# Performance work log

Measured on AMD Instinct MI355X. Metric: run time of the kernel, lower is better.

Reference implementation:

```python
import jax, jax.numpy as jnp
import numpy as np

N_DATA = 131072
N_HID = 32768
D = 256
E1 = 524288  # data -> hidden
E2 = 524288  # hidden -> hidden
E3 = 524288  # hidden -> data


def setup_inputs() -> dict:
    key = jax.random.key(0)
    ks = jax.random.split(key, 32)
    rn = lambda k, shape, s=0.05: (jax.random.normal(k, shape, jnp.float32) * s)
    inp = {
        "data_x": jax.random.normal(ks[0], (N_DATA, 8), jnp.float32),
        "hidden_x": jax.random.normal(ks[1], (N_HID, 3), jnp.float32),
        "dh_src": jax.random.randint(ks[2], (E1,), 0, N_DATA, jnp.int32),
        "dh_dst": jax.random.randint(ks[3], (E1,), 0, N_HID, jnp.int32),
        "hh_src": jax.random.randint(ks[4], (E2,), 0, N_HID, jnp.int32),
        "hh_dst": jax.random.randint(ks[5], (E2,), 0, N_HID, jnp.int32),
        "hd_src": jax.random.randint(ks[6], (E3,), 0, N_HID, jnp.int32),
        "hd_dst": jax.random.randint(ks[7], (E3,), 0, N_DATA, jnp.int32),
        # encoder params
        "enc_src_w": rn(ks[8], (D, 8)), "enc_src_b": rn(ks[9], (D,)),
        "enc_dst_w": rn(ks[10], (D, 3)), "enc_dst_b": rn(ks[11], (D,)),
        "enc_wl": rn(ks[12], (D, D)), "enc_bl": rn(ks[13], (D,)), "enc_wr": rn(ks[14], (D, D)),
        # processor params
        "proc_wl": rn(ks[15], (D, D)), "proc_bl": rn(ks[16], (D,)), "proc_wr": rn(ks[17], (D, D)),
        "proc_mlp_w": rn(ks[18], (D, D)), "proc_mlp_b": rn(ks[19], (D,)),
        # decoder params
        "dec_src_w": rn(ks[20], (D, D)), "dec_src_b": rn(ks[21], (D,)),
        "dec_dst_w": rn(ks[22], (D, 8)), "dec_dst_b": rn(ks[23], (D,)),
        "dec_wl": rn(ks[24], (D, D)), "dec_bl": rn(ks[25], (D,)), "dec_wr": rn(ks[26], (D, D)),
        "out_w": rn(ks[27], (8, D)), "out_b": rn(ks[28], (8,)),
    }
    return inp


def _gelu(x):
    return jax.nn.gelu(x, approximate=False)  # torch nn.GELU default (erf)


def _sage(x_src, x_dst, src, dst, wl, bl, wr, n_dst):
    """PyG SAGEConv, mean aggregation: lin_l(mean_j x_src[j]) + lin_r(x_dst)."""
    msg = x_src[src]                                              # [E, D] gather
    agg = jax.ops.segment_sum(msg, dst, num_segments=n_dst)       # [n_dst, D]
    cnt = jax.ops.segment_sum(jnp.ones((src.shape[0], 1), msg.dtype), dst,
                              num_segments=n_dst)
    mean = agg / jnp.maximum(cnt, 1.0)
    return mean @ wl.T + bl + x_dst @ wr.T


def reference(data_x, hidden_x, dh_src, dh_dst, hh_src, hh_dst, hd_src, hd_dst,
              enc_src_w, enc_src_b, enc_dst_w, enc_dst_b, enc_wl, enc_bl, enc_wr,
              proc_wl, proc_bl, proc_wr, proc_mlp_w, proc_mlp_b,
              dec_src_w, dec_src_b, dec_dst_w, dec_dst_b, dec_wl, dec_bl, dec_wr,
              out_w, out_b):
    # ---- encoder: data -> hidden ----
    h_data = _gelu(data_x @ enc_src_w.T + enc_src_b)
    h_hid = _gelu(hidden_x @ enc_dst_w.T + enc_dst_b)
    h_hid = _gelu(_sage(h_data, h_hid, dh_src, dh_dst, enc_wl, enc_bl, enc_wr, N_HID))
    # ---- processor: hidden -> hidden, then GELU-Linear-GELU MLP ----
    h_hid = _sage(h_hid, h_hid, hh_src, hh_dst, proc_wl, proc_bl, proc_wr, N_HID)
    h_hid = _gelu(_gelu(h_hid) @ proc_mlp_w.T + proc_mlp_b)
    # ---- decoder: hidden -> data ----
    s = _gelu(h_hid @ dec_src_w.T + dec_src_b)
    d = _gelu(data_x @ dec_dst_w.T + dec_dst_b)
    d = _gelu(_sage(s, d, hd_src, hd_dst, dec_wl, dec_bl, dec_wr, N_DATA))
    return d @ out_w.T + out_b  # [N_DATA, 8]
```

## Files before the change

kernel.cpp:

```cpp
#include <hip/hip_runtime.h>
#include <stdint.h>

#define NDATA 131072
#define NHID  32768
#define NEDGE 524288

typedef __bf16 bf16_t;
typedef __bf16 bf16x4 __attribute__((ext_vector_type(4)));
typedef __bf16 bf16x8 __attribute__((ext_vector_type(8)));
typedef float  f32x4  __attribute__((ext_vector_type(4)));

__device__ __forceinline__ float gelu_f(float x) {
    return 0.5f * x * (1.0f + erff(x * 0.7071067811865476f));
}

__device__ __forceinline__ void glds16(const void* g, void* l) {
    auto* gp = reinterpret_cast<const __attribute__((address_space(1))) uint32_t*>(
        reinterpret_cast<uintptr_t>(g));
    auto* lp = reinterpret_cast<__attribute__((address_space(3))) uint32_t*>(
        reinterpret_cast<uintptr_t>(l));
    __builtin_amdgcn_global_load_lds(gp, lp, 16, 0, 0);
}

struct WPtrs { const float* p[10]; };

__global__ __launch_bounds__(256)
void cvt_w_kernel(WPtrs wp, bf16_t* __restrict__ out) {
    const int i = blockIdx.x * 256 + threadIdx.x;
    if (i < 8 * 65536) {
        const int wsel = i >> 16, off = i & 65535;
        out[i] = (bf16_t)wp.p[wsel][off];
    } else if (i < 8 * 65536 + 2048) {
        out[i] = (bf16_t)wp.p[8][i - 8 * 65536];
    } else {
        out[i] = (bf16_t)wp.p[9][i - (8 * 65536 + 2048)];
    }
}

struct EdgePtrs { const int* src[3]; const int* dst[3]; };

__device__ __forceinline__ int cnt_off_of(int g) { return g == 0 ? 0 : (g == 1 ? NHID : 2 * NHID); }
__device__ __forceinline__ int rp_off_of(int g)  { return g == 0 ? 0 : (g == 1 ? NHID + 1 : 2 * NHID + 2); }
__device__ __forceinline__ int shift_of(int g)   { return g == 2 ? 10 : 8; }

__global__ __launch_bounds__(256)
void hist3(EdgePtrs ep, int* __restrict__ cnt_all) {
    const int g = blockIdx.x >> 11;
    const int i = ((blockIdx.x & 2047) << 8) + threadIdx.x;
    atomicAdd(&cnt_all[cnt_off_of(g) + ep.dst[g][i]], 1);
}

__global__ __launch_bounds__(256)
void scan_blk3(const int* __restrict__ cnt_all, int* __restrict__ pre_all,
               int* __restrict__ blk) {
    __shared__ int sh[256];
    const int bid = blockIdx.x;
    int g, local;
    if (bid < 32)      { g = 0; local = bid; }
    else if (bid < 64) { g = 1; local = bid - 32; }
    else               { g = 2; local = bid - 64; }
    const int t = threadIdx.x;
    const int cbase = cnt_off_of(g) + local * 1024 + t * 4;
    const int pbase = rp_off_of(g)  + local * 1024 + t * 4;
    int4 v = *(const int4*)(cnt_all + cbase);
    sh[t] = v.x + v.y + v.z + v.w;
    __syncthreads();
    for (int off = 1; off < 256; off <<= 1) {
        int other = 0;
        if (t >= off) other = sh[t - off];
        __syncthreads();
        if (t >= off) sh[t] += other;
        __syncthreads();
    }
    const int excl = (t == 0) ? 0 : sh[t - 1];
    int4 o;
    o.x = excl; o.y = o.x + v.x; o.z = o.y + v.y; o.w = o.z + v.z;
    *(int4*)(pre_all + pbase) = o;
    if (t == 255) blk[bid] = sh[255];
}

__global__ __launch_bounds__(256)
void scan_add3(const int* __restrict__ pre_all, const int* __restrict__ blk,
               int* __restrict__ rp_all, int* __restrict__ binA) {
    __shared__ int sh[256];
    const int bid = blockIdx.x;
    int g, local, gbase;
    if (bid < 32)      { g = 0; local = bid;      gbase = 0; }
    else if (bid < 64) { g = 1; local = bid - 32; gbase = 32; }
    else               { g = 2; local = bid - 64; gbase = 64; }
    const int t = threadIdx.x;
    int part = 0;
    if (t < local) part = blk[gbase + t];
    sh[t] = part;
    __syncthreads();
    for (int o2 = 128; o2 > 0; o2 >>= 1) {
        if (t < o2) sh[t] += sh[t + o2];
        __syncthreads();
    }
    const int off = sh[0];
    const int idx = local * 1024 + t * 4;
    const int pbase = rp_off_of(g) + idx;
    int4 v = *(const int4*)(pre_all + pbase);
    v.x += off; v.y += off; v.z += off; v.w += off;
    *(int4*)(rp_all + pbase) = v;
    const int bw = 1 << shift_of(g);
    if ((idx & (bw - 1)) == 0) binA[g * 128 + (idx >> shift_of(g))] = v.x;
    if (local == 0 && t == 0) {
        const int n = (g == 2) ? NDATA : NHID;
        rp_all[rp_off_of(g) + n] = NEDGE;
    }
}

__global__ __launch_bounds__(256)
void partition3(EdgePtrs ep, int* __restrict__ binA, int2* __restrict__ pairs) {
    __shared__ int hist[128], base[128], cur[128];
    const int g = blockIdx.x >> 7;
    const int blk = blockIdx.x & 127;
    const int t = threadIdx.x;
    const int shift = shift_of(g);
    const int e_base = blk * 4096;
    const int* src = ep.src[g];
    const int* dst = ep.dst[g];
    if (t < 128) { hist[t] = 0; cur[t] = 0; }
    __syncthreads();
    #pragma unroll
    for (int it = 0; it < 16; ++it) {
        const int d = dst[e_base + it * 256 + t];
        atomicAdd(&hist[d >> shift], 1);
    }
    __syncthreads();
    if (t < 128) base[t] = atomicAdd(&binA[g * 128 + t], hist[t]);
    __syncthreads();
    #pragma unroll
    for (int it = 0; it < 16; ++it) {
        const int e = e_base + it * 256 + t;
        const int s = src[e], d = dst[e];
        const int b = d >> shift;
        const int l = atomicAdd(&cur[b], 1);
        pairs[(size_t)g * NEDGE + base[b] + l] = make_int2(s, d);
    }
}

__global__ __launch_bounds__(256)
void binsort3(const int2* __restrict__ pairs, const int* __restrict__ rp_all,
              int* __restrict__ sorted_all) {
    __shared__ int cur[1024];
    const int g = blockIdx.x >> 7;
    const int b = blockIdx.x & 127;
    const int t = threadIdx.x;
    const int shift = shift_of(g);
    const int W = 1 << shift;
    const int d0 = b << shift;
    const int rpo = rp_off_of(g);
    for (int i = t; i < W; i += 256) cur[i] = rp_all[rpo + d0 + i];
    __syncthreads();
    const int e0 = rp_all[rpo + d0];
    const int e1 = rp_all[rpo + d0 + W];
    for (int e = e0 + t; e < e1; e += 256) {
        const int2 p = pairs[(size_t)g * NEDGE + e];
        const int pos = atomicAdd(&cur[p.y - d0], 1);
        sorted_all[(size_t)g * NEDGE + pos] = p.x;
    }
}

__global__ __launch_bounds__(256)
void csr_gather_mean(const bf16_t* __restrict__ feat, const int* __restrict__ row_ptr,
                     const int* __restrict__ sorted_src, bf16_t* __restrict__ mean, int n) {
    const int lane = threadIdx.x & 63;
    const int half = lane >> 5;
    const int col8 = (lane & 31) * 8;
    const int w = blockIdx.x * 4 + (threadIdx.x >> 6);
    if (w >= n) return;
    const int e0 = row_ptr[w], e1 = row_ptr[w + 1];
    float acc[8] = {0.f, 0.f, 0.f, 0.f, 0.f, 0.f, 0.f, 0.f};
    int e = e0 + half;
    for (; e + 2 < e1; e += 4) {
        const int s0 = sorted_src[e], s1 = sorted_src[e + 2];
        const bf16x8 v0 = *(const bf16x8*)(feat + (size_t)s0 * 256 + col8);
        const bf16x8 v1 = *(const bf16x8*)(feat + (size_t)s1 * 256 + col8);
        #pragma unroll
        for (int j = 0; j < 8; ++j) acc[j] += (float)v0[j] + (float)v1[j];
    }
    for (; e < e1; e += 2) {
        const int s0 = sorted_src[e];
        const bf16x8 v0 = *(const bf16x8*)(feat + (size_t)s0 * 256 + col8);
        #pragma unroll
        for (int j = 0; j < 8; ++j) acc[j] += (float)v0[j];
    }
    #pragma unroll
    for (int j = 0; j < 8; ++j) acc[j] += __shfl_xor(acc[j], 32, 64);
    if (half == 0) {
        const float ic = 1.0f / fmaxf((float)(e1 - e0), 1.0f);
        bf16x8 r;
        #pragma unroll
        for (int j = 0; j < 8; ++j) r[j] = (bf16_t)(acc[j] * ic);
        *(bf16x8*)(mean + (size_t)w * 256 + col8) = r;
    }
}

__global__ __launch_bounds__(256)
void enc_both(const float* __restrict__ hx, const float* __restrict__ w3,
              const float* __restrict__ b3, bf16_t* __restrict__ out3,
              const float* __restrict__ dx, const float* __restrict__ w8,
              const float* __restrict__ b8, bf16_t* __restrict__ out8) {
    __shared__ float ws[8 * 256];
    __shared__ float bs[256];
    const int t = threadIdx.x;
    const bool is8 = (blockIdx.x >= 512);
    if (is8) {
        #pragma unroll
        for (int j = 0; j < 8; ++j) ws[j * 256 + t] = w8[t * 8 + j];
        bs[t] = b8[t];
    } else {
        #pragma unroll
        for (int j = 0; j < 3; ++j) ws[j * 256 + t] = w3[t * 3 + j];
        bs[t] = b3[t];
    }
    __syncthreads();
    const int lane = t & 63, wv = t >> 6;
    const int f0 = lane * 4;
    const float4 b4 = *(const float4*)(&bs[f0]);
    if (!is8) {
        for (int node = blockIdx.x * 4 + wv; node < NHID; node += 512 * 4) {
            const float* xr = hx + (size_t)node * 3;
            float xv[3];
            #pragma unroll
            for (int j = 0; j < 3; ++j) xv[j] = xr[j];
            float a0 = b4.x, a1 = b4.y, a2 = b4.z, a3 = b4.w;
            #pragma unroll
            for (int j = 0; j < 3; ++j) {
                const float4 w4 = *(const float4*)(&ws[j * 256 + f0]);
                a0 += xv[j] * w4.x; a1 += xv[j] * w4.y;
                a2 += xv[j] * w4.z; a3 += xv[j] * w4.w;
            }
            bf16x4 r;
            r[0] = (bf16_t)gelu_f(a0); r[1] = (bf16_t)gelu_f(a1);
            r[2] = (bf16_t)gelu_f(a2); r[3] = (bf16_t)gelu_f(a3);
            *(bf16x4*)(out3 + (size_t)node * 256 + f0) = r;
        }
    } else {
        for (int node = (blockIdx.x - 512) * 4 + wv; node < NDATA; node += 2048 * 4) {
            const float* xr = dx + (size_t)node * 8;
            float xv[8];
            #pragma unroll
            for (int j = 0; j < 8; ++j) xv[j] = xr[j];
            float a0 = b4.x, a1 = b4.y, a2 = b4.z, a3 = b4.w;
            #pragma unroll
            for (int j = 0; j < 8; ++j) {
                const float4 w4 = *(const float4*)(&ws[j * 256 + f0]);
                a0 += xv[j] * w4.x; a1 += xv[j] * w4.y;
                a2 += xv[j] * w4.z; a3 += xv[j] * w4.w;
            }
            bf16x4 r;
            r[0] = (bf16_t)gelu_f(a0); r[1] = (bf16_t)gelu_f(a1);
            r[2] = (bf16_t)gelu_f(a2); r[3] = (bf16_t)gelu_f(a3);
            *(bf16x4*)(out8 + (size_t)node * 256 + f0) = r;
        }
    }
}

template<int DUAL>
__global__ __launch_bounds__(256, 4)
void mfma_gemm(const bf16_t* __restrict__ A1, const bf16_t* __restrict__ W1,
               const bf16_t* __restrict__ A2, const bf16_t* __restrict__ W2,
               const float* __restrict__ bias, bf16_t* __restrict__ C) {
    __shared__ bf16_t As[8 * 64 * 8];
    __shared__ bf16_t Bs[8 * 256 * 8];
    const int t = threadIdx.x;
    const int w = t >> 6, lane = t & 63;
    const int l15 = lane & 15, l4 = lane >> 4;
    const int m0 = blockIdx.x * 64;

    f32x4 acc[4][4];
    #pragma unroll
    for (int nb = 0; nb < 4; ++nb) {
        const float bv = bias[w * 64 + nb * 16 + l15];
        #pragma unroll
        for (int m = 0; m < 4; ++m) {
            acc[m][nb][0] = bv; acc[m][nb][1] = bv; acc[m][nb][2] = bv; acc[m][nb][3] = bv;
        }
    }

    #pragma unroll
    for (int p = 0; p <= DUAL; ++p) {
        const bf16_t* Ap = p ? A2 : A1;
        const bf16_t* Wp = p ? W2 : W1;
        for (int kt = 0; kt < 4; ++kt) {
            const int k0 = kt * 64;
            __syncthreads();
            glds16(Ap + (size_t)(m0 + lane) * 256 + k0 + w * 8, &As[(w * 64) * 8]);
            glds16(Ap + (size_t)(m0 + lane) * 256 + k0 + (w + 4) * 8, &As[((w + 4) * 64) * 8]);
            #pragma unroll
            for (int q = 0; q < 8; ++q)
                glds16(Wp + (size_t)(w * 64 + lane) * 256 + k0 + q * 8,
                       &Bs[(q * 256 + w * 64) * 8]);
            __syncthreads();
            #pragma unroll
            for (int h = 0; h < 2; ++h) {
                bf16x8 af[4], bfr[4];
                #pragma unroll
                for (int m = 0; m < 4; ++m)
                    af[m] = *(const bf16x8*)(&As[((h * 4 + l4) * 64 + m * 16 + l15) * 8]);
                #pragma unroll
                for (int nb = 0; nb < 4; ++nb)
                    bfr[nb] = *(const bf16x8*)(&Bs[((h * 4 + l4) * 256 + w * 64 + nb * 16 + l15) * 8]);
                #pragma unroll
                for (int m = 0; m < 4; ++m)
                    #pragma unroll
                    for (int nb = 0; nb < 4; ++nb)
                        acc[m][nb] = __builtin_amdgcn_mfma_f32_16x16x32_bf16(af[m], bfr[nb], acc[m][nb], 0, 0, 0);
            }
        }
    }

    #pragma unroll
    for (int m = 0; m < 4; ++m) {
        #pragma unroll
        for (int nb = 0; nb < 4; ++nb) {
            const int col = w * 64 + nb * 16 + l15;
            #pragma unroll
            for (int i = 0; i < 4; ++i) {
                const int row = m0 + m * 16 + l4 * 4 + i;
                C[(size_t)row * 256 + col] = (bf16_t)gelu_f(acc[m][nb][i]);
            }
        }
    }
}

__global__ __launch_bounds__(256, 4)
void dec_gemm(const bf16_t* __restrict__ A1, const bf16_t* __restrict__ W1,
              const float* __restrict__ xdat, const bf16_t* __restrict__ wdb,
              const float* __restrict__ bd, const bf16_t* __restrict__ W2,
              const float* __restrict__ bias, const bf16_t* __restrict__ owb,
              const float* __restrict__ ob, float* __restrict__ out) {
    __shared__ __align__(16) char smem[40960];
    bf16_t* As   = (bf16_t*)smem;
    bf16_t* Bs   = (bf16_t*)(smem + 8192);
    bf16_t* tt   = (bf16_t*)smem;
    float*  part = (float*)(smem + 16384);

    const int t = threadIdx.x;
    const int w = t >> 6, lane = t & 63;
    const int l15 = lane & 15, l4 = lane >> 4;
    const int m0 = blockIdx.x * 64;

    bf16x8 af_x;
    #pragma unroll
    for (int j = 0; j < 8; ++j) af_x[j] = (bf16_t)0.0f;
    if (l4 == 0) {
        const float* xrp = xdat + (size_t)(m0 + w * 16 + l15) * 8;
        const float4 xa = *(const float4*)(xrp);
        const float4 xb = *(const float4*)(xrp + 4);
        af_x[0] = (bf16_t)xa.x; af_x[1] = (bf16_t)xa.y; af_x[2] = (bf16_t)xa.z; af_x[3] = (bf16_t)xa.w;
        af_x[4] = (bf16_t)xb.x; af_x[5] = (bf16_t)xb.y; af_x[6] = (bf16_t)xb.z; af_x[7] = (bf16_t)xb.w;
    }

    f32x4 acc[4][4];
    #pragma unroll
    for (int nb = 0; nb < 4; ++nb) {
        const float bv = bias[w * 64 + nb * 16 + l15];
        #pragma unroll
        for (int m = 0; m < 4; ++m) {
            acc[m][nb][0] = bv; acc[m][nb][1] = bv; acc[m][nb][2] = bv; acc[m][nb][3] = bv;
        }
    }

    #pragma unroll
    for (int p = 0; p < 2; ++p) {
        const bf16_t* Wp = p ? W2 : W1;
        for (int kt = 0; kt < 4; ++kt) {
            const int k0 = kt * 64;
            __syncthreads();
            if (p == 0) {
                glds16(A1 + (size_t)(m0 + lane) * 256 + k0 + w * 8, &As[(w * 64) * 8]);
                glds16(A1 + (size_t)(m0 + lane) * 256 + k0 + (w + 4) * 8, &As[((w + 4) * 64) * 8]);
            } else {
                #pragma unroll
                for (int nb2 = 0; nb2 < 4; ++nb2) {
                    const int cl = nb2 * 16 + l15;
                    const int col = k0 + cl;
                    f32x4 ad;
                    const float bv = bd[col];
                    ad[0] = bv; ad[1] = bv; ad[2] = bv; ad[3] = bv;
                    bf16x8 bf_d;
                    #pragma unroll
                    for (int j = 0; j < 8; ++j) bf_d[j] = (bf16_t)0.0f;
                    if (l4 == 0) bf_d = *(const bf16x8*)(wdb + col * 8);
                    ad = __builtin_amdgcn_mfma_f32_16x16x32_bf16(af_x, bf_d, ad, 0, 0, 0);
                    const int kq = cl >> 3, jj = cl & 7;
                    #pragma unroll
                    for (int i = 0; i < 4; ++i)
                        As[(kq * 64 + w * 16 + l4 * 4 + i) * 8 + jj] = (bf16_t)gelu_f(ad[i]);
                }
            }
            #pragma unroll
            for (int q = 0; q < 8; ++q)
                glds16(Wp + (size_t)(w * 64 + lane) * 256 + k0 + q * 8,
                       &Bs[(q * 256 + w * 64) * 8]);
            __syncthreads();
            #pragma unroll
            for (int h = 0; h < 2; ++h) {
                bf16x8 af[4], bfr[4];
                #pragma unroll
                for (int m = 0; m < 4; ++m)
                    af[m] = *(const bf16x8*)(&As[((h * 4 + l4) * 64 + m * 16 + l15) * 8]);
                #pragma unroll
                for (int nb = 0; nb < 4; ++nb)
                    bfr[nb] = *(const bf16x8*)(&Bs[((h * 4 + l4) * 256 + w * 64 + nb * 16 + l15) * 8]);
                #pragma unroll
                for (int m = 0; m < 4; ++m)
                    #pragma unroll
                    for (int nb = 0; nb < 4; ++nb)
                        acc[m][nb] = __builtin_amdgcn_mfma_f32_16x16x32_bf16(af[m], bfr[nb], acc[m][nb], 0, 0, 0);
            }
        }
    }

    __syncthreads();

    bf16x8 owf[2];
    #pragma unroll
    for (int s = 0; s < 2; ++s) {
        #pragma unroll
        for (int j = 0; j < 8; ++j) owf[s][j] = (bf16_t)0.0f;
        if (l15 < 8)
            owf[s] = *(const bf16x8*)(owb + l15 * 256 + w * 64 + s * 32 + l4 * 8);
    }

    bf16_t* ttw = tt + w * 2048;
    #pragma unroll
    for (int h = 0; h < 2; ++h) {
        #pragma unroll
        for (int mm = 0; mm < 2; ++mm) {
            const int m = h * 2 + mm;
            #pragma unroll
            for (int nb = 0; nb < 4; ++nb) {
                const int col = nb * 16 + l15;
                const int kg = col >> 3, cj = col & 7;
                #pragma unroll
                for (int i = 0; i < 4; ++i) {
                    const int rl = mm * 16 + l4 * 4 + i;
                    ttw[(kg * 32 + rl) * 8 + cj] = (bf16_t)gelu_f(acc[m][nb][i]);
                }
            }
        }
        f32x4 accp[2];
        #pragma unroll
        for (int mb = 0; mb < 2; ++mb) {
            accp[mb][0] = 0.f; accp[mb][1] = 0.f; accp[mb][2] = 0.f; accp[mb][3] = 0.f;
            #pragma unroll
            for (int s = 0; s < 2; ++s) {
                const bf16x8 af = *(const bf16x8*)(&ttw[((s * 4 + l4) * 32 + mb * 16 + l15) * 8]);
                accp[mb] = __builtin_amdgcn_mfma_f32_16x16x32_bf16(af, owf[s], accp[mb], 0, 0, 0);
            }
        }
        __syncthreads();
        #pragma unroll
        for (int mb = 0; mb < 2; ++mb)
            #pragma unroll
            for (int i = 0; i < 4; ++i)
                part[(w * 32 + mb * 16 + l4 * 4 + i) * 16 + l15] = accp[mb][i];
        __syncthreads();
        {
            const int row = t >> 3, o = t & 7;
            const float v = part[(0 * 32 + row) * 16 + o] + part[(1 * 32 + row) * 16 + o]
                          + part[(2 * 32 + row) * 16 + o] + part[(3 * 32 + row) * 16 + o] + ob[o];
            out[(size_t)(m0 + h * 32 + row) * 8 + o] = v;
        }
    }
}


extern "C" void kernel_launch(void* const* d_in, const int* in_sizes, int n_in,
                              void* d_out, int out_size, void* d_ws, size_t ws_size,
                              hipStream_t stream) {
    const float* data_x   = (const float*)d_in[0];
    const float* hidden_x = (const float*)d_in[1];
    const int* dh_src = (const int*)d_in[2];
    const int* dh_dst = (const int*)d_in[3];
    const int* hh_src = (const int*)d_in[4];
    const int* hh_dst = (const int*)d_in[5];
    const int* hd_src = (const int*)d_in[6];
    const int* hd_dst = (const int*)d_in[7];
    const float* enc_src_w = (const float*)d_in[8];
    const float* enc_src_b = (const float*)d_in[9];
    const float* enc_dst_w = (const float*)d_in[10];
    const float* enc_dst_b = (const float*)d_in[11];
    const float* enc_wl = (const float*)d_in[12];
    const float* enc_bl = (const float*)d_in[13];
    const float* enc_wr = (const float*)d_in[14];
    const float* proc_wl = (const float*)d_in[15];
    const float* proc_bl = (const float*)d_in[16];
    const float* proc_wr = (const float*)d_in[17];
    const float* proc_mlp_w = (const float*)d_in[18];
    const float* proc_mlp_b = (const float*)d_in[19];
    const float* dec_src_w = (const float*)d_in[20];
    const float* dec_src_b = (const float*)d_in[21];
    const float* dec_dst_w = (const float*)d_in[22];
    const float* dec_dst_b = (const float*)d_in[23];
    const float* dec_wl = (const float*)d_in[24];
    const float* dec_bl = (const float*)d_in[25];
    const float* dec_wr = (const float*)d_in[26];
    const float* out_w  = (const float*)d_in[27];
    const float* out_b  = (const float*)d_in[28];
    float* out = (float*)d_out;

    bf16_t* h_a   = (bf16_t*)d_ws;
    bf16_t* h_b   = h_a + (size_t)NHID * 256;
    bf16_t* h_msg = h_b + (size_t)NHID * 256;
    bf16_t* dmean = h_msg + (size_t)NDATA * 256;
    bf16_t* wbuf  = dmean + (size_t)NDATA * 256;
    int* cnt_all    = (int*)(wbuf + 8 * 65536 + 4096);
    int* rp_all     = cnt_all + (2 * NHID + NDATA);
    int* sorted_all = rp_all + (2 * NHID + NDATA + 3);
    int* blk_sums   = sorted_all + (size_t)3 * NEDGE;
    int* binA       = blk_sums + 192;
    int2* pairs     = (int2*)(((uintptr_t)(binA + 384) + 15) & ~(uintptr_t)15);

    bf16_t* W_enc_wl  = wbuf + 0 * 65536;
    bf16_t* W_enc_wr  = wbuf + 1 * 65536;
    bf16_t* W_proc_wl = wbuf + 2 * 65536;
    bf16_t* W_proc_wr = wbuf + 3 * 65536;
    bf16_t* W_mlp     = wbuf + 4 * 65536;
    bf16_t* W_dec_src = wbuf + 5 * 65536;
    bf16_t* W_dec_wl  = wbuf + 6 * 65536;
    bf16_t* W_dec_wr  = wbuf + 7 * 65536;
    bf16_t* W_out     = wbuf + 8 * 65536;
    bf16_t* W_dd      = wbuf + 8 * 65536 + 2048;

    const int* rp_dh = rp_all;
    const int* rp_hh = rp_all + NHID + 1;
    const int* rp_hd = rp_all + 2 * NHID + 2;
    const int* so_dh = sorted_all;
    const int* so_hh = sorted_all + NEDGE;
    const int* so_hd = sorted_all + 2 * (size_t)NEDGE;

    WPtrs wp;
    wp.p[0] = enc_wl;  wp.p[1] = enc_wr;  wp.p[2] = proc_wl; wp.p[3] = proc_wr;
    wp.p[4] = proc_mlp_w; wp.p[5] = dec_src_w; wp.p[6] = dec_wl; wp.p[7] = dec_wr;
    wp.p[8] = out_w; wp.p[9] = dec_dst_w;
    cvt_w_kernel<<<2064, 256, 0, stream>>>(wp, wbuf);

    EdgePtrs ep;
    ep.src[0] = dh_src; ep.dst[0] = dh_dst;
    ep.src[1] = hh_src; ep.dst[1] = hh_dst;
    ep.src[2] = hd_src; ep.dst[2] = hd_dst;
    hipMemsetAsync(cnt_all, 0, (size_t)(2 * NHID + NDATA) * sizeof(int), stream);
    hist3<<<3 * 2048, 256, 0, stream>>>(ep, cnt_all);
    scan_blk3<<<192, 256, 0, stream>>>(cnt_all, rp_all, blk_sums);
    scan_add3<<<192, 256, 0, stream>>>(rp_all, blk_sums, rp_all, binA);
    partition3<<<3 * 128, 256, 0, stream>>>(ep, binA, pairs);
    binsort3<<<3 * 128, 256, 0, stream>>>(pairs, rp_all, sorted_all);

    enc_both<<<2560, 256, 0, stream>>>(hidden_x, enc_dst_w, enc_dst_b, h_a,
                                       data_x, enc_src_w, enc_src_b, h_msg);
    csr_gather_mean<<<NHID / 4, 256, 0, stream>>>(h_msg, rp_dh, so_dh, h_b, NHID);
    mfma_gemm<1><<<NHID / 64, 256, 0, stream>>>(h_b, W_enc_wl, h_a, W_enc_wr, enc_bl, h_b);

    csr_gather_mean<<<NHID / 4, 256, 0, stream>>>(h_b, rp_hh, so_hh, h_a, NHID);
    mfma_gemm<1><<<NHID / 64, 256, 0, stream>>>(h_a, W_proc_wl, h_b, W_proc_wr, proc_bl, h_a);
    mfma_gemm<0><<<NHID / 64, 256, 0, stream>>>(h_a, W_mlp, nullptr, nullptr, proc_mlp_b, h_b);
    mfma_gemm<0><<<NHID / 64, 256, 0, stream>>>(h_b, W_dec_src, nullptr, nullptr, dec_src_b, h_a);

    csr_gather_mean<<<NDATA / 4, 256, 0, stream>>>(h_a, rp_hd, so_hd, dmean, NDATA);
    dec_gemm<<<NDATA / 64, 256, 0, stream>>>(dmean, W_dec_wl, data_x, W_dd, dec_dst_b,
                                             W_dec_wr, dec_bl, W_out, out_b, out);
}
```

Measured before the change: 482.9 us.

## Drop block barriers in MFMA GEMMs via wave-private weight staging and direct A loads

The GEMM kernels now load A fragments straight from global memory into registers. Each wave stages only its own weight slice in LDS with a per-wave vmcnt fence, which removes the per-step __syncthreads. mfma_gemm halves its row tile to 32 so twice as many blocks launch, and uses a 32-wide K step. dec_gemm precomputes the whole data_x encoder tile into LDS up front instead of per K step, at the cost of more shared memory and occupancy lowered to 3. Without block barriers, the in-place GEMMs (C aliasing A1) can race: one wave may write output rows while another wave is still reading them.

```diff
diff --git a/kernel.cpp b/kernel.cpp
--- a/kernel.cpp
+++ b/kernel.cpp
@@ -20,6 +20,11 @@
     auto* lp = reinterpret_cast<__attribute__((address_space(3))) uint32_t*>(
         reinterpret_cast<uintptr_t>(l));
     __builtin_amdgcn_global_load_lds(gp, lp, 16, 0, 0);
+}
+
+__device__ __forceinline__ void wave_vm_fence() {
+    asm volatile("s_waitcnt vmcnt(0)" ::: "memory");
+    __builtin_amdgcn_sched_barrier(0);
 }
 
 struct WPtrs { const float* p[10]; };
@@ -264,19 +269,18 @@
 void mfma_gemm(const bf16_t* __restrict__ A1, const bf16_t* __restrict__ W1,
                const bf16_t* __restrict__ A2, const bf16_t* __restrict__ W2,
                const float* __restrict__ bias, bf16_t* __restrict__ C) {
-    __shared__ bf16_t As[8 * 64 * 8];
-    __shared__ bf16_t Bs[8 * 256 * 8];
+    __shared__ bf16_t Bs[4 * 256 * 8];
     const int t = threadIdx.x;
     const int w = t >> 6, lane = t & 63;
     const int l15 = lane & 15, l4 = lane >> 4;
-    const int m0 = blockIdx.x * 64;
-
-    f32x4 acc[4][4];
+    const int m0 = blockIdx.x * 32;
+
+    f32x4 acc[2][4];
     #pragma unroll
     for (int nb = 0; nb < 4; ++nb) {
         const float bv = bias[w * 64 + nb * 16 + l15];
         #pragma unroll
-        for (int m = 0; m < 4; ++m) {
+        for (int m = 0; m < 2; ++m) {
             acc[m][nb][0] = bv; acc[m][nb][1] = bv; acc[m][nb][2] = bv; acc[m][nb][3] = bv;
         }
     }
@@ -285,36 +289,32 @@
     for (int p = 0; p <= DUAL; ++p) {
         const bf16_t* Ap = p ? A2 : A1;
         const bf16_t* Wp = p ? W2 : W1;
-        for (int kt = 0; kt < 4; ++kt) {
-            const int k0 = kt * 64;
-            __syncthreads();
-            glds16(Ap + (size_t)(m0 + lane) * 256 + k0 + w * 8, &As[(w * 64) * 8]);
-            glds16(Ap + (size_t)(m0 + lane) * 256 + k0 + (w + 4) * 8, &As[((w + 4) * 64) * 8]);
-            #pragma unroll
-            for (int q = 0; q < 8; ++q)
+        for (int kt = 0; kt < 8; ++kt) {
+            const int k0 = kt * 32;
+            __builtin_amdgcn_sched_barrier(0);
+            #pragma unroll
+            for (int q = 0; q < 4; ++q)
                 glds16(Wp + (size_t)(w * 64 + lane) * 256 + k0 + q * 8,
                        &Bs[(q * 256 + w * 64) * 8]);
-            __syncthreads();
-            #pragma unroll
-            for (int h = 0; h < 2; ++h) {
-                bf16x8 af[4], bfr[4];
-                #pragma unroll
-                for (int m = 0; m < 4; ++m)
-                    af[m] = *(const bf16x8*)(&As[((h * 4 + l4) * 64 + m * 16 + l15) * 8]);
+            bf16x8 af[2];
+            #pragma unroll
+            for (int m = 0; m < 2; ++m)
+                af[m] = *(const bf16x8*)(Ap + (size_t)(m0 + m * 16 + l15) * 256 + k0 + l4 * 8);
+            wave_vm_fence();
+            bf16x8 bfr[4];
+            #pragma unroll
+            for (int nb = 0; nb < 4; ++nb)
+                bfr[nb] = *(const bf16x8*)(&Bs[(l4 * 256 + w * 64 + nb * 16 + l15) * 8]);
+            #pragma unroll
+            for (int m = 0; m < 2; ++m)
                 #pragma unroll
                 for (int nb = 0; nb < 4; ++nb)
-                    bfr[nb] = *(const bf16x8*)(&Bs[((h * 4 + l4) * 256 + w * 64 + nb * 16 + l15) * 8]);
-                #pragma unroll
-                for (int m = 0; m < 4; ++m)
-                    #pragma unroll
-                    for (int nb = 0; nb < 4; ++nb)
-                        acc[m][nb] = __builtin_amdgcn_mfma_f32_16x16x32_bf16(af[m], bfr[nb], acc[m][nb], 0, 0, 0);
-            }
-        }
-    }
-
-    #pragma unroll
-    for (int m = 0; m < 4; ++m) {
+                    acc[m][nb] = __builtin_amdgcn_mfma_f32_16x16x32_bf16(af[m], bfr[nb], acc[m][nb], 0, 0, 0);
+        }
+    }
+
+    #pragma unroll
+    for (int m = 0; m < 2; ++m) {
         #pragma unroll
         for (int nb = 0; nb < 4; ++nb) {
             const int col = w * 64 + nb * 16 + l15;
@@ -327,15 +327,15 @@
     }
 }
 
-__global__ __launch_bounds__(256, 4)
+__global__ __launch_bounds__(256, 3)
 void dec_gemm(const bf16_t* __restrict__ A1, const bf16_t* __restrict__ W1,
               const float* __restrict__ xdat, const bf16_t* __restrict__ wdb,
               const float* __restrict__ bd, const bf16_t* __restrict__ W2,
               const float* __restrict__ bias, const bf16_t* __restrict__ owb,
               const float* __restrict__ ob, float* __restrict__ out) {
-    __shared__ __align__(16) char smem[40960];
-    bf16_t* As   = (bf16_t*)smem;
-    bf16_t* Bs   = (bf16_t*)(smem + 8192);
+    __shared__ __align__(16) char smem[49152];
+    bf16_t* dL = (bf16_t*)smem;
+    bf16_t* Bs = (bf16_t*)(smem + 32768);
     bf16_t* tt   = (bf16_t*)smem;
     float*  part = (float*)(smem + 16384);
 
@@ -344,15 +344,33 @@
     const int l15 = lane & 15, l4 = lane >> 4;
     const int m0 = blockIdx.x * 64;
 
-    bf16x8 af_x;
-    #pragma unroll
-    for (int j = 0; j < 8; ++j) af_x[j] = (bf16_t)0.0f;
-    if (l4 == 0) {
-        const float* xrp = xdat + (size_t)(m0 + w * 16 + l15) * 8;
-        const float4 xa = *(const float4*)(xrp);
-        const float4 xb = *(const float4*)(xrp + 4);
-        af_x[0] = (bf16_t)xa.x; af_x[1] = (bf16_t)xa.y; af_x[2] = (bf16_t)xa.z; af_x[3] = (bf16_t)xa.w;
-        af_x[4] = (bf16_t)xb.x; af_x[5] = (bf16_t)xb.y; af_x[6] = (bf16_t)xb.z; af_x[7] = (bf16_t)xb.w;
+    {
+        bf16x8 af_x;
+        #pragma unroll
+        for (int j = 0; j < 8; ++j) af_x[j] = (bf16_t)0.0f;
+        if (l4 == 0) {
+            const float* xrp = xdat + (size_t)(m0 + w * 16 + l15) * 8;
+            const float4 xa = *(const float4*)(xrp);
+            const float4 xb = *(const float4*)(xrp + 4);
+            af_x[0] = (bf16_t)xa.x; af_x[1] = (bf16_t)xa.y; af_x[2] = (bf16_t)xa.z; af_x[3] = (bf16_t)xa.w;
+            af_x[4] = (bf16_t)xb.x; af_x[5] = (bf16_t)xb.y; af_x[6] = (bf16_t)xb.z; af_x[7] = (bf16_t)xb.w;
+        }
+        #pragma unroll
+        for (int cb = 0; cb < 16; ++cb) {
+            const int col = cb * 16 + l15;
+            f32x4 ad;
+            const float bv = bd[col];
+            ad[0] = bv; ad[1] = bv; ad[2] = bv; ad[3] = bv;
+            bf16x8 bf_d;
+            #pragma unroll
+            for (int j = 0; j < 8; ++j) bf_d[j] = (bf16_t)0.0f;
+            if (l4 == 0) bf_d = *(const bf16x8*)(wdb + col * 8);
+            ad = __builtin_amdgcn_mfma_f32_16x16x32_bf16(af_x, bf_d, ad, 0, 0, 0);
+            const int kq = col >> 3, jj = col & 7;
+            #pragma unroll
+            for (int i = 0; i < 4; ++i)
+                dL[(kq * 64 + w * 16 + l4 * 4 + i) * 8 + jj] = (bf16_t)gelu_f(ad[i]);
+        }
     }
 
     f32x4 acc[4][4];
@@ -364,55 +382,38 @@
             acc[m][nb][0] = bv; acc[m][nb][1] = bv; acc[m][nb][2] = bv; acc[m][nb][3] = bv;
         }
     }
+    __syncthreads();
 
     #pragma unroll
     for (int p = 0; p < 2; ++p) {
         const bf16_t* Wp = p ? W2 : W1;
-        for (int kt = 0; kt < 4; ++kt) {
-            const int k0 = kt * 64;
-            __syncthreads();
+        for (int kt = 0; kt < 8; ++kt) {
+            const int k0 = kt * 32;
+            __builtin_amdgcn_sched_barrier(0);
+            #pragma unroll
+            for (int q = 0; q < 4; ++q)
+                glds16(Wp + (size_t)(w * 64 + lane) * 256 + k0 + q * 8,
+                       &Bs[(q * 256 + w * 64) * 8]);
+            bf16x8 af[4];
             if (p == 0) {
-                glds16(A1 + (size_t)(m0 + lane) * 256 + k0 + w * 8, &As[(w * 64) * 8]);
-                glds16(A1 + (size_t)(m0 + lane) * 256 + k0 + (w + 4) * 8, &As[((w + 4) * 64) * 8]);
+                #pragma unroll
+                for (int m = 0; m < 4; ++m)
+                    af[m] = *(const bf16x8*)(A1 + (size_t)(m0 + m * 16 + l15) * 256 + k0 + l4 * 8);
             } else {
                 #pragma unroll
-                for (int nb2 = 0; nb2 < 4; ++nb2) {
-                    const int cl = nb2 * 16 + l15;
-                    const int col = k0 + cl;
-                    f32x4 ad;
-                    const float bv = bd[col];
-                    ad[0] = bv; ad[1] = bv; ad[2] = bv; ad[3] = bv;
-                    bf16x8 bf_d;
-                    #pragma unroll
-                    for (int j = 0; j < 8; ++j) bf_d[j] = (bf16_t)0.0f;
-                    if (l4 == 0) bf_d = *(const bf16x8*)(wdb + col * 8);
-                    ad = __builtin_amdgcn_mfma_f32_16x16x32_bf16(af_x, bf_d, ad, 0, 0, 0);
-                    const int kq = cl >> 3, jj = cl & 7;
-                    #pragma unroll
-                    for (int i = 0; i < 4; ++i)
-                        As[(kq * 64 + w * 16 + l4 * 4 + i) * 8 + jj] = (bf16_t)gelu_f(ad[i]);
-                }
+                for (int m = 0; m < 4; ++m)
+                    af[m] = *(const bf16x8*)(&dL[((kt * 4 + l4) * 64 + m * 16 + l15) * 8]);
             }
-            #pragma unroll
-            for (int q = 0; q < 8; ++q)
-                glds16(Wp + (size_t)(w * 64 + lane) * 256 + k0 + q * 8,
-                       &Bs[(q * 256 + w * 64) * 8]);
-            __syncthreads();
-            #pragma unroll
-            for (int h = 0; h < 2; ++h) {
-                bf16x8 af[4], bfr[4];
-                #pragma unroll
-                for (int m = 0; m < 4; ++m)
-                    af[m] = *(const bf16x8*)(&As[((h * 4 + l4) * 64 + m * 16 + l15) * 8]);
+            wave_vm_fence();
+            bf16x8 bfr[4];
+            #pragma unroll
+            for (int nb = 0; nb < 4; ++nb)
+                bfr[nb] = *(const bf16x8*)(&Bs[(l4 * 256 + w * 64 + nb * 16 + l15) * 8]);
+            #pragma unroll
+            for (int m = 0; m < 4; ++m)
                 #pragma unroll
                 for (int nb = 0; nb < 4; ++nb)
-                    bfr[nb] = *(const bf16x8*)(&Bs[((h * 4 + l4) * 256 + w * 64 + nb * 16 + l15) * 8]);
-                #pragma unroll
-                for (int m = 0; m < 4; ++m)
-                    #pragma unroll
-                    for (int nb = 0; nb < 4; ++nb)
-                        acc[m][nb] = __builtin_amdgcn_mfma_f32_16x16x32_bf16(af[m], bfr[nb], acc[m][nb], 0, 0, 0);
-            }
+                    acc[m][nb] = __builtin_amdgcn_mfma_f32_16x16x32_bf16(af[m], bfr[nb], acc[m][nb], 0, 0, 0);
         }
     }
 
@@ -555,12 +556,12 @@
     enc_both<<<2560, 256, 0, stream>>>(hidden_x, enc_dst_w, enc_dst_b, h_a,
                                        data_x, enc_src_w, enc_src_b, h_msg);
     csr_gather_mean<<<NHID / 4, 256, 0, stream>>>(h_msg, rp_dh, so_dh, h_b, NHID);
-    mfma_gemm<1><<<NHID / 64, 256, 0, stream>>>(h_b, W_enc_wl, h_a, W_enc_wr, enc_bl, h_b);
+    mfma_gemm<1><<<NHID / 32, 256, 0, stream>>>(h_b, W_enc_wl, h_a, W_enc_wr, enc_bl, h_b);
 
     csr_gather_mean<<<NHID / 4, 256, 0, stream>>>(h_b, rp_hh, so_hh, h_a, NHID);
-    mfma_gemm<1><<<NHID / 64, 256, 0, stream>>>(h_a, W_proc_wl, h_b, W_proc_wr, proc_bl, h_a);
-    mfma_gemm<0><<<NHID / 64, 256, 0, stream>>>(h_a, W_mlp, nullptr, nullptr, proc_mlp_b, h_b);
-    mfma_gemm<0><<<NHID / 64, 256, 0, stream>>>(h_b, W_dec_src, nullptr, nullptr, dec_src_b, h_a);
+    mfma_gemm<1><<<NHID / 32, 256, 0, stream>>>(h_a, W_proc_wl, h_b, W_proc_wr, proc_bl, h_a);
+    mfma_gemm<0><<<NHID / 32, 256, 0, stream>>>(h_a, W_mlp, nullptr, nullptr, proc_mlp_b, h_b);
+    mfma_gemm<0><<<NHID / 32, 256, 0, stream>>>(h_b, W_dec_src, nullptr, nullptr, dec_src_b, h_a);
 
     csr_gather_mean<<<NDATA / 4, 256, 0, stream>>>(h_a, rp_hd, so_hd, dmean, NDATA);
     dec_gemm<<<NDATA / 64, 256, 0, stream>>>(dmean, W_dec_wl, data_x, W_dd, dec_dst_b,
```

Measured after the change: 553.9 us. +14.7%, slower.
